# Optimization experiments

Measured on AMD Instinct MI355X. Metric: run time of the kernel, lower is better.

The kernel has to match this reference:

```python
import jax, jax.numpy as jnp
import numpy as np

D_MODEL = 1024
N_HEADS = 16
HEAD_DIM = D_MODEL // N_HEADS  # 64
BATCH = 2
SEQ = 2048
THETA = 10000.0


def _rope_tables(theta, d_k, max_seq_len):
    # matches RoPE.__init__: d = theta**(2*arange(d_k//2)/d_k); t = s / d
    inv = theta ** (2.0 * jnp.arange(0, d_k // 2, dtype=jnp.float32) / d_k)  # [d_k//2]
    s = jnp.arange(max_seq_len, dtype=jnp.float32)[:, None]  # [S,1]
    t = s / inv[None, :]  # [S, d_k//2]
    return jnp.sin(t), jnp.cos(t)


def setup_inputs() -> dict:
    key = jax.random.key(0)
    ks = jax.random.split(key, 5)
    std = np.sqrt(2.0 / (D_MODEL + D_MODEL))
    x = jax.random.normal(ks[0], (BATCH, SEQ, D_MODEL), dtype=jnp.float32)
    Wq = jax.random.normal(ks[1], (D_MODEL, D_MODEL), dtype=jnp.float32) * std
    Wk = jax.random.normal(ks[2], (D_MODEL, D_MODEL), dtype=jnp.float32) * std
    Wv = jax.random.normal(ks[3], (D_MODEL, D_MODEL), dtype=jnp.float32) * std
    Wo = jax.random.normal(ks[4], (D_MODEL, D_MODEL), dtype=jnp.float32) * std
    token_positions = jnp.arange(SEQ, dtype=jnp.int64)
    rope_sin, rope_cos = _rope_tables(THETA, HEAD_DIM, SEQ)
    return {"x": x, "token_positions": token_positions, "Wq": Wq, "Wk": Wk,
            "Wv": Wv, "Wo": Wo, "rope_sin": rope_sin, "rope_cos": rope_cos}


def _apply_rope(x, sin, cos):
    # x: [B, H, S, d_k]; sin/cos: [S, d_k//2] (gathered by token_positions)
    x1 = x[..., ::2]
    x2 = x[..., 1::2]
    x_even = x1 * cos - x2 * sin
    x_odd = x1 * sin + x2 * cos
    # interleave back: stack on last dim then flatten
    return jnp.stack([x_even, x_odd], axis=-1).reshape(x.shape)


def reference(x, token_positions, Wq, Wk, Wv, Wo, rope_sin, rope_cos):
    b, s, _ = x.shape
    h, d = N_HEADS, HEAD_DIM

    def proj(W):
        y = jnp.einsum('oi,bsi->bso', W, x)
        return y.reshape(b, s, h, d).transpose(0, 2, 1, 3)  # [b, h, s, d]

    q = proj(Wq)
    k = proj(Wk)
    v = proj(Wv)

    sin = rope_sin[token_positions]  # [s, d//2]
    cos = rope_cos[token_positions]
    q = _apply_rope(q, sin, cos)
    k = _apply_rope(k, sin, cos)

    # causal scaled-dot-product attention (FlashAttention.apply(..., True))
    scale = 1.0 / jnp.sqrt(jnp.asarray(d, dtype=x.dtype))
    scores = jnp.einsum('bhqd,bhkd->bhqk', q, k) * scale
    causal = jnp.tril(jnp.ones((s, s), dtype=bool))
    scores = jnp.where(causal, scores, jnp.finfo(x.dtype).min)
    attn = jax.nn.softmax(scores, axis=-1)
    out = jnp.einsum('bhqk,bhkd->bhqd', attn, v)  # [b, h, s, d]
    out = out.transpose(0, 2, 1, 3).reshape(b, s, h * d)
    return jnp.einsum('oi,bsi->bso', Wo, out)
```

## Files before the change

kernel.cpp:

```cpp
#include <hip/hip_runtime.h>
#include <hip/hip_bf16.h>
#include <math.h>

#define BATCH   2
#define S_LEN   2048
#define DM      1024
#define NH      16
#define HD      64
#define MROWS   4096

typedef __hip_bfloat16 bf16;
typedef __attribute__((ext_vector_type(8))) short short8;
typedef __attribute__((ext_vector_type(4))) float float4v;

#define QSCALE 0.18033688011112043f

__device__ __forceinline__ short f2s(float x) {
    union { bf16 h; short s; } u; u.h = __float2bfloat16(x); return u.s;
}
__device__ __forceinline__ short8 load8(const void* p) {
    return *reinterpret_cast<const short8*>(p);
}
__device__ __forceinline__ void cvt8(const float* g, bf16* d) {
    float4v a = *reinterpret_cast<const float4v*>(g);
    float4v b = *reinterpret_cast<const float4v*>(g + 4);
    short8 r;
    r[0] = f2s(a[0]); r[1] = f2s(a[1]); r[2] = f2s(a[2]); r[3] = f2s(a[3]);
    r[4] = f2s(b[0]); r[5] = f2s(b[1]); r[6] = f2s(b[2]); r[7] = f2s(b[3]);
    *reinterpret_cast<short8*>(d) = r;
}
__device__ __forceinline__ void gll16(const void* g, void* l) {
    __builtin_amdgcn_global_load_lds(
        (const __attribute__((address_space(1))) unsigned int*)g,
        (__attribute__((address_space(3))) unsigned int*)l,
        16, 0, 0);
}
__device__ __forceinline__ unsigned pack2(float a, float b) {
    union { float f; unsigned u; } ua, ub;
    ua.f = a; ub.f = b;
    return ((ua.u + 0x8000u) >> 16) | ((ub.u + 0x8000u) & 0xFFFF0000u);
}

__global__ __launch_bounds__(256) void cvt_kernel(const float* __restrict__ x,
                                                  const float* __restrict__ wq,
                                                  const float* __restrict__ wk,
                                                  const float* __restrict__ wv,
                                                  const float* __restrict__ wo,
                                                  bf16* __restrict__ xb,
                                                  bf16* __restrict__ wqb,
                                                  bf16* __restrict__ wkb,
                                                  bf16* __restrict__ wvb,
                                                  bf16* __restrict__ wob) {
    const size_t i = ((size_t)blockIdx.x * 256 + threadIdx.x) * 8;
    const size_t NX = (size_t)MROWS * DM;
    const size_t NW = (size_t)DM * DM;
    if (i < NX)                { cvt8(x  + i,               xb  + i); }
    else if (i < NX + NW)      { cvt8(wq + (i - NX),        wqb + (i - NX)); }
    else if (i < NX + 2 * NW)  { cvt8(wk + (i - NX - NW),   wkb + (i - NX - NW)); }
    else if (i < NX + 3 * NW)  { cvt8(wv + (i - NX - 2*NW), wvb + (i - NX - 2*NW)); }
    else                       { cvt8(wo + (i - NX - 3*NW), wob + (i - NX - 3*NW)); }
}

__global__ __launch_bounds__(256) void qkv_gemm(const bf16* __restrict__ A,
                                                const bf16* __restrict__ Wqb,
                                                const bf16* __restrict__ Wkb,
                                                const bf16* __restrict__ Wvb,
                                                bf16* __restrict__ Qb, bf16* __restrict__ Kb,
                                                bf16* __restrict__ Vtb,
                                                const float* __restrict__ rsin,
                                                const float* __restrict__ rcos) {
    __shared__ short As[128 * 64];
    __shared__ short Bs[128 * 64];

    const int j    = threadIdx.x;
    const int w    = j >> 6;
    const int lane = j & 63;
    const int quad = lane >> 4;
    const int lid  = lane & 15;
    const int wm   = w & 1, wn = w >> 1;

    const int mb  = blockIdx.x * 128;
    const int sel = blockIdx.y >> 3;
    const int nb  = (blockIdx.y & 7) * 128;
    const bf16* W = (sel == 0) ? Wqb : (sel == 1) ? Wkb : Wvb;

    int sOff[4];
#pragma unroll
    for (int i = 0; i < 4; ++i) {
        const int idx = (i * 4 + w) * 64 + lane;
        const int r = idx >> 3, c = (idx & 7) ^ (r & 7);
        sOff[i] = r * DM + c * 8;
    }

    float4v acc[4][4] = {};
    for (int k0 = 0; k0 < DM; k0 += 64) {
#pragma unroll
        for (int i = 0; i < 4; ++i)
            gll16(A + (size_t)mb * DM + k0 + sOff[i], &As[(i * 4 + w) * 512]);
#pragma unroll
        for (int i = 0; i < 4; ++i)
            gll16(W + (size_t)nb * DM + k0 + sOff[i], &Bs[(i * 4 + w) * 512]);
        __syncthreads();
#pragma unroll
        for (int ks = 0; ks < 2; ++ks) {
            short8 af[4], bfr[4];
#pragma unroll
            for (int mt = 0; mt < 4; ++mt)
                af[mt] = load8(&As[(wm * 64 + mt * 16 + lid) * 64 + (((ks * 4 + quad) ^ (lid & 7)) * 8)]);
#pragma unroll
            for (int nt = 0; nt < 4; ++nt)
                bfr[nt] = load8(&Bs[(wn * 64 + nt * 16 + lid) * 64 + (((ks * 4 + quad) ^ (lid & 7)) * 8)]);
#pragma unroll
            for (int mt = 0; mt < 4; ++mt)
#pragma unroll
                for (int nt = 0; nt < 4; ++nt)
                    acc[mt][nt] = __builtin_amdgcn_mfma_f32_16x16x32_bf16(af[mt], bfr[nt], acc[mt][nt], 0, 0, 0);
        }
        __syncthreads();
    }

#pragma unroll
    for (int mt = 0; mt < 4; ++mt) {
#pragma unroll
        for (int nt = 0; nt < 4; ++nt) {
            const int n = nb + wn * 64 + nt * 16 + lid;
            const int h = n >> 6, d = n & 63;
#pragma unroll
            for (int r = 0; r < 4; ++r) {
                const int m = mb + wm * 64 + mt * 16 + quad * 4 + r;
                const int s = m & (S_LEN - 1), bi = m >> 11;
                float val = acc[mt][nt][r];
                if (sel == 0) val *= QSCALE;
                float par = __shfl_xor(val, 1, 64);
                if (sel == 2) {
                    Vtb[(((size_t)bi * NH + h) * HD + d) * S_LEN + s] = __float2bfloat16(val);
                } else {
                    const float sn = rsin[s * 32 + (d >> 1)];
                    const float cs = rcos[s * 32 + (d >> 1)];
                    const float v = ((d & 1) == 0) ? val * cs - par * sn
                                                   : par * sn + val * cs;
                    bf16* dst = (sel == 0) ? Qb : Kb;
                    dst[(((size_t)bi * NH + h) * S_LEN + s) * HD + d] = __float2bfloat16(v);
                }
            }
        }
    }
}

__global__ __launch_bounds__(256) void out_gemm(const bf16* __restrict__ A,
                                                const bf16* __restrict__ W,
                                                float* __restrict__ out) {
    __shared__ short As[128 * 64];
    __shared__ short Bs[64 * 64];

    const int j    = threadIdx.x;
    const int w    = j >> 6;
    const int lane = j & 63;
    const int quad = lane >> 4;
    const int lid  = lane & 15;

    const int mb = blockIdx.x * 128;
    const int nb = blockIdx.y * 64;

    int aOff[4], bOff[2];
#pragma unroll
    for (int i = 0; i < 4; ++i) {
        const int idx = (i * 4 + w) * 64 + lane;
        const int r = idx >> 3, c = (idx & 7) ^ (r & 7);
        aOff[i] = r * DM + c * 8;
    }
#pragma unroll
    for (int i = 0; i < 2; ++i) {
        const int idx = (i * 4 + w) * 64 + lane;
        const int r = idx >> 3, c = (idx & 7) ^ (r & 7);
        bOff[i] = r * DM + c * 8;
    }

    float4v acc[2][4] = {};
    for (int k0 = 0; k0 < DM; k0 += 64) {
#pragma unroll
        for (int i = 0; i < 4; ++i)
            gll16(A + (size_t)mb * DM + k0 + aOff[i], &As[(i * 4 + w) * 512]);
#pragma unroll
        for (int i = 0; i < 2; ++i)
            gll16(W + (size_t)nb * DM + k0 + bOff[i], &Bs[(i * 4 + w) * 512]);
        __syncthreads();
#pragma unroll
        for (int ks = 0; ks < 2; ++ks) {
            short8 af[2], bfr[4];
#pragma unroll
            for (int mt = 0; mt < 2; ++mt)
                af[mt] = load8(&As[(w * 32 + mt * 16 + lid) * 64 + (((ks * 4 + quad) ^ (lid & 7)) * 8)]);
#pragma unroll
            for (int nt = 0; nt < 4; ++nt)
                bfr[nt] = load8(&Bs[(nt * 16 + lid) * 64 + (((ks * 4 + quad) ^ (lid & 7)) * 8)]);
#pragma unroll
            for (int mt = 0; mt < 2; ++mt)
#pragma unroll
                for (int nt = 0; nt < 4; ++nt)
                    acc[mt][nt] = __builtin_amdgcn_mfma_f32_16x16x32_bf16(af[mt], bfr[nt], acc[mt][nt], 0, 0, 0);
        }
        __syncthreads();
    }

#pragma unroll
    for (int mt = 0; mt < 2; ++mt)
#pragma unroll
        for (int nt = 0; nt < 4; ++nt) {
            const int n = nb + nt * 16 + lid;
#pragma unroll
            for (int r = 0; r < 4; ++r) {
                const int m = mb + w * 32 + mt * 16 + quad * 4 + r;
                out[(size_t)m * DM + n] = acc[mt][nt][r];
            }
        }
}

__global__ __launch_bounds__(256) void flash5(const bf16* __restrict__ Q,
                                              const bf16* __restrict__ K,
                                              const bf16* __restrict__ Vt,
                                              bf16* __restrict__ att) {
    __shared__ short Ks[128 * 64];
    __shared__ short Vs[64 * 128];
    __shared__ short Pb[128 * 128];

    const int j    = threadIdx.x;
    const int w    = j >> 6;
    const int lane = j & 63;
    const int quad = lane >> 4;
    const int lid  = lane & 15;
    const int bh   = blockIdx.x;
    const int by   = blockIdx.y;
    const int qt   = (by < 8) ? (15 - by) : (by - 8);
    const int bi   = bh >> 4, h = bh & 15;
    const int qb   = qt * 128;

    const size_t bh_off = (size_t)bh * S_LEN * HD;
    const bf16* Qp = Q + bh_off;
    const bf16* Kp = K + bh_off;
    const bf16* Vp = Vt + bh_off;

    short8 aQ[2][2];
#pragma unroll
    for (int mm = 0; mm < 2; ++mm)
#pragma unroll
        for (int kf = 0; kf < 2; ++kf)
            aQ[mm][kf] = load8(Qp + (size_t)(qb + w * 32 + mm * 16 + lid) * HD + kf * 32 + quad * 8);

    int kOff[4], vOff[4];
#pragma unroll
    for (int i = 0; i < 4; ++i) {
        const int idx = (i * 4 + w) * 64 + lane;
        const int kr = idx >> 3, kc = (idx & 7) ^ (kr & 7);
        kOff[i] = kr * HD + kc * 8;
        const int vr = idx >> 4, vc = (idx & 15) ^ (vr & 15);
        vOff[i] = vr * S_LEN + vc * 8;
    }

    float4v accO[2][4] = {};
    float4v accS[2] = {};
    short8 ones;
#pragma unroll
    for (int t = 0; t < 8; ++t) ones[t] = (short)0x3F80;

    const int nkt = qt + 1;
    for (int kti = 0; kti < nkt; ++kti) {
        const int kt = kti * 128;
        __syncthreads();
#pragma unroll
        for (int i = 0; i < 4; ++i)
            gll16(Kp + (size_t)kt * HD + kOff[i], &Ks[(i * 4 + w) * 512]);
#pragma unroll
        for (int i = 0; i < 4; ++i)
            gll16(Vp + kt + vOff[i], &Vs[(i * 4 + w) * 512]);
        __syncthreads();

        const bool diag = (kti == nkt - 1);

#pragma unroll
        for (int nt = 0; nt < 8; ++nt) {
            const int krow = nt * 16 + lid;
            short8 aK0 = load8(&Ks[krow * 64 + ((quad       ^ (lid & 7)) * 8)]);
            short8 aK1 = load8(&Ks[krow * 64 + (((4 + quad) ^ (lid & 7)) * 8)]);
#pragma unroll
            for (int mm = 0; mm < 2; ++mm) {
                float4v z = {};
                z = __builtin_amdgcn_mfma_f32_16x16x32_bf16(aK0, aQ[mm][0], z, 0, 0, 0);
                z = __builtin_amdgcn_mfma_f32_16x16x32_bf16(aK1, aQ[mm][1], z, 0, 0, 0);
                if (diag) {
                    const int qcol = qb + w * 32 + mm * 16 + lid;
#pragma unroll
                    for (int r = 0; r < 4; ++r)
                        if (kt + nt * 16 + quad * 4 + r > qcol) z[r] = -1e30f;
                }
                const float p0 = __builtin_amdgcn_exp2f(z[0]);
                const float p1 = __builtin_amdgcn_exp2f(z[1]);
                const float p2 = __builtin_amdgcn_exp2f(z[2]);
                const float p3 = __builtin_amdgcn_exp2f(z[3]);
                const int qrow = w * 32 + mm * 16 + lid;
                const int unit = (nt * 4 + quad) ^ ((lid & 7) * 2);
                uint2 pkd; pkd.x = pack2(p0, p1); pkd.y = pack2(p2, p3);
                *reinterpret_cast<uint2*>(&Pb[qrow * 128 + unit * 4]) = pkd;
            }
        }

        short8 aP[2][4];
#pragma unroll
        for (int mm = 0; mm < 2; ++mm) {
            const int qrow = w * 32 + mm * 16 + lid;
#pragma unroll
            for (int g = 0; g < 4; ++g) {
                const int u = (g * 8 + quad * 2) ^ ((lid & 7) * 2);
                aP[mm][g] = load8(&Pb[qrow * 128 + u * 4]);
                accS[mm] = __builtin_amdgcn_mfma_f32_16x16x32_bf16(aP[mm][g], ones, accS[mm], 0, 0, 0);
            }
        }
#pragma unroll
        for (int dt = 0; dt < 4; ++dt) {
#pragma unroll
            for (int g = 0; g < 4; ++g) {
                short8 bV = load8(&Vs[(dt * 16 + lid) * 128 + (((g * 4 + quad) ^ lid) * 8)]);
#pragma unroll
                for (int mm = 0; mm < 2; ++mm)
                    accO[mm][dt] = __builtin_amdgcn_mfma_f32_16x16x32_bf16(aP[mm][g], bV, accO[mm][dt], 0, 0, 0);
            }
        }
    }

#pragma unroll
    for (int mm = 0; mm < 2; ++mm) {
#pragma unroll
        for (int r = 0; r < 4; ++r) {
            const float inv = 1.0f / accS[mm][r];
            const int q = qb + w * 32 + mm * 16 + quad * 4 + r;
#pragma unroll
            for (int dt = 0; dt < 4; ++dt) {
                const int d = dt * 16 + lid;
                att[((size_t)bi * S_LEN + q) * DM + h * HD + d] =
                    __float2bfloat16(accO[mm][dt][r] * inv);
            }
        }
    }
}

extern "C" void kernel_launch(void* const* d_in, const int* in_sizes, int n_in,
                              void* d_out, int out_size, void* d_ws, size_t ws_size,
                              hipStream_t stream) {
    const float* x    = (const float*)d_in[0];
    const float* Wq   = (const float*)d_in[2];
    const float* Wk   = (const float*)d_in[3];
    const float* Wv   = (const float*)d_in[4];
    const float* Wo   = (const float*)d_in[5];
    const float* rsin = (const float*)d_in[6];
    const float* rcos = (const float*)d_in[7];
    float* out = (float*)d_out;

    char* ws = (char*)d_ws;
    const size_t MB = 1024 * 1024;
    bf16* Qb  = (bf16*)(ws + 0 * MB);
    bf16* Kb  = (bf16*)(ws + 8 * MB);
    bf16* Vtb = (bf16*)(ws + 16 * MB);
    bf16* xb  = (bf16*)(ws + 24 * MB);
    bf16* Wqb = (bf16*)(ws + 32 * MB);
    bf16* Wkb = (bf16*)(ws + 34 * MB);
    bf16* Wvb = (bf16*)(ws + 36 * MB);
    bf16* Wob = (bf16*)(ws + 38 * MB);
    bf16* atb = xb;

    cvt_kernel<<<4096, 256, 0, stream>>>(x, Wq, Wk, Wv, Wo, xb, Wqb, Wkb, Wvb, Wob);
    qkv_gemm<<<dim3(MROWS / 128, 24), 256, 0, stream>>>(xb, Wqb, Wkb, Wvb, Qb, Kb, Vtb, rsin, rcos);
    flash5<<<dim3(BATCH * NH, 16), 256, 0, stream>>>(Qb, Kb, Vtb, atb);
    out_gemm<<<dim3(MROWS / 128, DM / 64), 256, 0, stream>>>(atb, Wob, out);
}
```

Measured before the change: 212.7 us.

## Double-buffer GEMM LDS tiles and register-prefetch K/V in flash attention

The QKV and output GEMMs now keep two LDS buffers. The next k-tile is issued through global_load_lds before computing on the current one, using explicit vmcnt waits and raw barriers in place of __syncthreads. The flash kernel replaces direct global-to-LDS loads with register prefetch: the next K/V tile is loaded into registers while the current one is stored to LDS and consumed. The goal is to hide global memory latency behind MFMA work, at the cost of doubled LDS in the GEMMs (lower occupancy) and more VGPRs in the flash kernel. The hand-written waitcnt encodings and barrier ordering carry a correctness risk.

```diff
diff --git a/kernel.cpp b/kernel.cpp
--- a/kernel.cpp
+++ b/kernel.cpp
@@ -14,6 +14,11 @@
 typedef __attribute__((ext_vector_type(4))) float float4v;
 
 #define QSCALE 0.18033688011112043f
+
+#define WC_VM0   0x0F70
+#define WC_VM6   0x0F76
+#define WC_VM8   0x0F78
+#define WC_LGKM0 0xC07F
 
 __device__ __forceinline__ short f2s(float x) {
     union { bf16 h; short s; } u; u.h = __float2bfloat16(x); return u.s;
@@ -69,8 +74,8 @@
                                                 bf16* __restrict__ Vtb,
                                                 const float* __restrict__ rsin,
                                                 const float* __restrict__ rcos) {
-    __shared__ short As[128 * 64];
-    __shared__ short Bs[128 * 64];
+    __shared__ short As[2][128 * 64];
+    __shared__ short Bs[2][128 * 64];
 
     const int j    = threadIdx.x;
     const int w    = j >> 6;
@@ -91,32 +96,47 @@
         const int r = idx >> 3, c = (idx & 7) ^ (r & 7);
         sOff[i] = r * DM + c * 8;
     }
+    const bf16* baseA = A + (size_t)mb * DM;
+    const bf16* baseB = W + (size_t)nb * DM;
+
+#pragma unroll
+    for (int i = 0; i < 4; ++i) gll16(baseA + sOff[i], &As[0][(i * 4 + w) * 512]);
+#pragma unroll
+    for (int i = 0; i < 4; ++i) gll16(baseB + sOff[i], &Bs[0][(i * 4 + w) * 512]);
 
     float4v acc[4][4] = {};
-    for (int k0 = 0; k0 < DM; k0 += 64) {
-#pragma unroll
-        for (int i = 0; i < 4; ++i)
-            gll16(A + (size_t)mb * DM + k0 + sOff[i], &As[(i * 4 + w) * 512]);
-#pragma unroll
-        for (int i = 0; i < 4; ++i)
-            gll16(W + (size_t)nb * DM + k0 + sOff[i], &Bs[(i * 4 + w) * 512]);
-        __syncthreads();
+#pragma unroll 2
+    for (int it = 0; it < 16; ++it) {
+        __builtin_amdgcn_s_barrier();
+        if (it < 15) {
+            const int k0 = (it + 1) * 64, b = (it + 1) & 1;
+#pragma unroll
+            for (int i = 0; i < 4; ++i) gll16(baseA + k0 + sOff[i], &As[b][(i * 4 + w) * 512]);
+#pragma unroll
+            for (int i = 0; i < 4; ++i) gll16(baseB + k0 + sOff[i], &Bs[b][(i * 4 + w) * 512]);
+            __builtin_amdgcn_s_waitcnt(WC_VM8);
+        } else {
+            __builtin_amdgcn_s_waitcnt(WC_VM0);
+        }
+        __builtin_amdgcn_s_barrier();
+
+        const short* as = As[it & 1];
+        const short* bs = Bs[it & 1];
 #pragma unroll
         for (int ks = 0; ks < 2; ++ks) {
             short8 af[4], bfr[4];
 #pragma unroll
             for (int mt = 0; mt < 4; ++mt)
-                af[mt] = load8(&As[(wm * 64 + mt * 16 + lid) * 64 + (((ks * 4 + quad) ^ (lid & 7)) * 8)]);
+                af[mt] = load8(&as[(wm * 64 + mt * 16 + lid) * 64 + (((ks * 4 + quad) ^ (lid & 7)) * 8)]);
 #pragma unroll
             for (int nt = 0; nt < 4; ++nt)
-                bfr[nt] = load8(&Bs[(wn * 64 + nt * 16 + lid) * 64 + (((ks * 4 + quad) ^ (lid & 7)) * 8)]);
+                bfr[nt] = load8(&bs[(wn * 64 + nt * 16 + lid) * 64 + (((ks * 4 + quad) ^ (lid & 7)) * 8)]);
 #pragma unroll
             for (int mt = 0; mt < 4; ++mt)
 #pragma unroll
                 for (int nt = 0; nt < 4; ++nt)
                     acc[mt][nt] = __builtin_amdgcn_mfma_f32_16x16x32_bf16(af[mt], bfr[nt], acc[mt][nt], 0, 0, 0);
         }
-        __syncthreads();
     }
 
 #pragma unroll
@@ -150,8 +170,8 @@
 __global__ __launch_bounds__(256) void out_gemm(const bf16* __restrict__ A,
                                                 const bf16* __restrict__ W,
                                                 float* __restrict__ out) {
-    __shared__ short As[128 * 64];
-    __shared__ short Bs[64 * 64];
+    __shared__ short As[2][128 * 64];
+    __shared__ short Bs[2][64 * 64];
 
     const int j    = threadIdx.x;
     const int w    = j >> 6;
@@ -175,32 +195,47 @@
         const int r = idx >> 3, c = (idx & 7) ^ (r & 7);
         bOff[i] = r * DM + c * 8;
     }
+    const bf16* baseA = A + (size_t)mb * DM;
+    const bf16* baseB = W + (size_t)nb * DM;
+
+#pragma unroll
+    for (int i = 0; i < 4; ++i) gll16(baseA + aOff[i], &As[0][(i * 4 + w) * 512]);
+#pragma unroll
+    for (int i = 0; i < 2; ++i) gll16(baseB + bOff[i], &Bs[0][(i * 4 + w) * 512]);
 
     float4v acc[2][4] = {};
-    for (int k0 = 0; k0 < DM; k0 += 64) {
-#pragma unroll
-        for (int i = 0; i < 4; ++i)
-            gll16(A + (size_t)mb * DM + k0 + aOff[i], &As[(i * 4 + w) * 512]);
-#pragma unroll
-        for (int i = 0; i < 2; ++i)
-            gll16(W + (size_t)nb * DM + k0 + bOff[i], &Bs[(i * 4 + w) * 512]);
-        __syncthreads();
+#pragma unroll 2
+    for (int it = 0; it < 16; ++it) {
+        __builtin_amdgcn_s_barrier();
+        if (it < 15) {
+            const int k0 = (it + 1) * 64, b = (it + 1) & 1;
+#pragma unroll
+            for (int i = 0; i < 4; ++i) gll16(baseA + k0 + aOff[i], &As[b][(i * 4 + w) * 512]);
+#pragma unroll
+            for (int i = 0; i < 2; ++i) gll16(baseB + k0 + bOff[i], &Bs[b][(i * 4 + w) * 512]);
+            __builtin_amdgcn_s_waitcnt(WC_VM6);
+        } else {
+            __builtin_amdgcn_s_waitcnt(WC_VM0);
+        }
+        __builtin_amdgcn_s_barrier();
+
+        const short* as = As[it & 1];
+        const short* bs = Bs[it & 1];
 #pragma unroll
         for (int ks = 0; ks < 2; ++ks) {
             short8 af[2], bfr[4];
 #pragma unroll
             for (int mt = 0; mt < 2; ++mt)
-                af[mt] = load8(&As[(w * 32 + mt * 16 + lid) * 64 + (((ks * 4 + quad) ^ (lid & 7)) * 8)]);
+                af[mt] = load8(&as[(w * 32 + mt * 16 + lid) * 64 + (((ks * 4 + quad) ^ (lid & 7)) * 8)]);
 #pragma unroll
             for (int nt = 0; nt < 4; ++nt)
-                bfr[nt] = load8(&Bs[(nt * 16 + lid) * 64 + (((ks * 4 + quad) ^ (lid & 7)) * 8)]);
+                bfr[nt] = load8(&bs[(nt * 16 + lid) * 64 + (((ks * 4 + quad) ^ (lid & 7)) * 8)]);
 #pragma unroll
             for (int mt = 0; mt < 2; ++mt)
 #pragma unroll
                 for (int nt = 0; nt < 4; ++nt)
                     acc[mt][nt] = __builtin_amdgcn_mfma_f32_16x16x32_bf16(af[mt], bfr[nt], acc[mt][nt], 0, 0, 0);
         }
-        __syncthreads();
     }
 
 #pragma unroll
@@ -216,7 +251,7 @@
         }
 }
 
-__global__ __launch_bounds__(256) void flash5(const bf16* __restrict__ Q,
+__global__ __launch_bounds__(256) void flash6(const bf16* __restrict__ Q,
                                               const bf16* __restrict__ K,
                                               const bf16* __restrict__ Vt,
                                               bf16* __restrict__ att) {
@@ -263,18 +298,32 @@
 #pragma unroll
     for (int t = 0; t < 8; ++t) ones[t] = (short)0x3F80;
 
+    short8 kReg[4], vReg[4];
+#pragma unroll
+    for (int i = 0; i < 4; ++i) kReg[i] = load8(Kp + kOff[i]);
+#pragma unroll
+    for (int i = 0; i < 4; ++i) vReg[i] = load8(Vp + vOff[i]);
+
     const int nkt = qt + 1;
     for (int kti = 0; kti < nkt; ++kti) {
+        __builtin_amdgcn_s_barrier();
+#pragma unroll
+        for (int i = 0; i < 4; ++i)
+            *reinterpret_cast<short8*>(&Ks[(i * 4 + w) * 512 + lane * 8]) = kReg[i];
+#pragma unroll
+        for (int i = 0; i < 4; ++i)
+            *reinterpret_cast<short8*>(&Vs[(i * 4 + w) * 512 + lane * 8]) = vReg[i];
+        if (kti + 1 < nkt) {
+            const int ktn = (kti + 1) * 128;
+#pragma unroll
+            for (int i = 0; i < 4; ++i) kReg[i] = load8(Kp + (size_t)ktn * HD + kOff[i]);
+#pragma unroll
+            for (int i = 0; i < 4; ++i) vReg[i] = load8(Vp + ktn + vOff[i]);
+        }
+        __builtin_amdgcn_s_waitcnt(WC_LGKM0);
+        __builtin_amdgcn_s_barrier();
+
         const int kt = kti * 128;
-        __syncthreads();
-#pragma unroll
-        for (int i = 0; i < 4; ++i)
-            gll16(Kp + (size_t)kt * HD + kOff[i], &Ks[(i * 4 + w) * 512]);
-#pragma unroll
-        for (int i = 0; i < 4; ++i)
-            gll16(Vp + kt + vOff[i], &Vs[(i * 4 + w) * 512]);
-        __syncthreads();
-
         const bool diag = (kti == nkt - 1);
 
 #pragma unroll
@@ -369,6 +418,6 @@
 
     cvt_kernel<<<4096, 256, 0, stream>>>(x, Wq, Wk, Wv, Wo, xb, Wqb, Wkb, Wvb, Wob);
     qkv_gemm<<<dim3(MROWS / 128, 24), 256, 0, stream>>>(xb, Wqb, Wkb, Wvb, Qb, Kb, Vtb, rsin, rcos);
-    flash5<<<dim3(BATCH * NH, 16), 256, 0, stream>>>(Qb, Kb, Vtb, atb);
+    flash6<<<dim3(BATCH * NH, 16), 256, 0, stream>>>(Qb, Kb, Vtb, atb);
     out_gemm<<<dim3(MROWS / 128, DM / 64), 256, 0, stream>>>(atb, Wob, out);
 }
```

Result: faster. 199.7 us (-6.1%).
